# Optimization experiments

Hardware: AMD Instinct MI355X
Metric: run time of the kernel (lower is better)

The kernel has to match this reference:

```python
import jax, jax.numpy as jnp
import numpy as np

N, L, H, E, D = 8, 1024, 16, 1024, 64  # batch, seq_len, heads, embed_size, head_dim


def _xavier(k, shape):
    fan_out, fan_in = shape
    lim = np.sqrt(6.0 / (fan_in + fan_out)).astype(np.float32)
    return jax.random.uniform(k, shape, jnp.float32, -lim, lim)


def setup_inputs() -> dict:
    key = jax.random.key(0)
    ks = jax.random.split(key, 6)
    return {
        "x": jax.random.normal(ks[0], (N, L, E, 1), jnp.float32),
        "Wq": _xavier(ks[1], (D, D)), "bq": jnp.zeros((D,), jnp.float32),
        "Wk": _xavier(ks[2], (D, D)), "bk": jnp.zeros((D,), jnp.float32),
        "Wv": _xavier(ks[3], (D, D)), "bv": jnp.zeros((D,), jnp.float32),
        "Erel": jax.random.normal(ks[4], (1, L, D), jnp.float32),
        "Wo": _xavier(ks[5], (E, E)), "bo": jnp.zeros((E,), jnp.float32),
    }


def _skew(qe):
    # qe: [N, H, L, L] -> pad one zero col on the left, reshape, drop first row
    n, h, l, _ = qe.shape
    p = jnp.pad(qe, ((0, 0), (0, 0), (0, 0), (1, 0)))  # [N,H,L,L+1]
    p = p.reshape(n, h, l + 1, l)
    return p[:, :, 1:, :]  # [N,H,L,L]


def reference(x, Wq, bq, Wk, bk, Wv, bv, Erel, Wo, bo):
    x0 = x[:, :, :, 0]                      # [N, L, E]
    z = x0.reshape(N, L, H, D)              # [N, L, H, D]
    q = z @ Wq.T + bq
    k = z @ Wk.T + bk
    v = z @ Wv.T + bv
    # QE = queries.transpose(1,2) @ E.transpose(1,2): [N,H,L,D] @ [D,L] -> [N,H,L,L]
    QE = jnp.einsum('nlhd,td->nhlt', q, Erel[0])
    # mask_positions: zero where triu(ones,1).flip(1) == 1
    mask = jnp.flip(jnp.triu(jnp.ones((L, L), jnp.float32), 1), axis=1)
    QE = jnp.where(mask == 1, 0.0, QE)
    S = _skew(QE)                           # [N,H,L,L]
    qk = jnp.einsum('nqhd,nkhd->nhqk', q, k)
    attention = jax.nn.softmax(qk / jnp.sqrt(jnp.float32(E)), axis=3) + S
    out = jnp.einsum('nhql,nlhd->nqhd', attention, v).reshape(N, L, H * D)
    return out @ Wo.T + bo                  # [N, L, E]
```

## Files before the change

### kernel.cpp

```cpp
#include <hip/hip_runtime.h>
#include <math.h>

#define N_ 8
#define L_ 1024
#define H_ 16
#define E_ 1024
#define D_ 64

typedef __bf16 bf16x8 __attribute__((ext_vector_type(8)));
typedef __bf16 bf16x4 __attribute__((ext_vector_type(4)));
typedef float  f32x4  __attribute__((ext_vector_type(4)));

#define MFMA16(a, b, c) __builtin_amdgcn_mfma_f32_16x16x32_bf16((a), (b), (c), 0, 0, 0)

#define KSCALE 0.04508422002778011f

__global__ __launch_bounds__(256) void prep_kernel(
    const float* __restrict__ Wo, const float* __restrict__ Erel,
    __bf16* __restrict__ wobf, __bf16* __restrict__ erbf)
{
    const int idx = blockIdx.x * 256 + threadIdx.x;
    const float* src;
    __bf16* dst;
    int off;
    if (blockIdx.x < 1024) { src = Wo;   dst = wobf; off = idx * 4; }
    else                   { src = Erel; dst = erbf; off = (idx - 1024 * 256) * 4; }
    const float4 f = *(const float4*)(src + off);
    bf16x4 h;
    h[0] = (__bf16)f.x; h[1] = (__bf16)f.y; h[2] = (__bf16)f.z; h[3] = (__bf16)f.w;
    *(bf16x4*)(dst + off) = h;
}

__global__ __launch_bounds__(256) void qkv_kernel(
    const float* __restrict__ x,
    const float* __restrict__ Wq, const float* __restrict__ bq,
    const float* __restrict__ Wk, const float* __restrict__ bk,
    const float* __restrict__ Wv, const float* __restrict__ bv,
    __bf16* __restrict__ qo, __bf16* __restrict__ ko, __bf16* __restrict__ vo)
{
    const int t = threadIdx.x, w = t >> 6, lane = t & 63;
    const int quad = lane >> 4, l16 = lane & 15;
    const int m0 = blockIdx.x * 64;

    __shared__ __bf16 xs[64][72];
    __shared__ __bf16 wls[3][64][72];

    #pragma unroll
    for (int i = 0; i < 4; ++i) {
        const int idx = t + i * 256, row = idx >> 4, c4 = idx & 15;
        {
            const float4 f = *(const float4*)(x + (size_t)(m0 + row) * 64 + c4 * 4);
            bf16x4 hh; hh[0]=(__bf16)f.x; hh[1]=(__bf16)f.y; hh[2]=(__bf16)f.z; hh[3]=(__bf16)f.w;
            *(bf16x4*)&xs[row][c4 * 4] = hh;
        }
        {
            const float4 f = *(const float4*)(Wq + (size_t)row * 64 + c4 * 4);
            bf16x4 hh; hh[0]=(__bf16)f.x; hh[1]=(__bf16)f.y; hh[2]=(__bf16)f.z; hh[3]=(__bf16)f.w;
            *(bf16x4*)&wls[0][row][c4 * 4] = hh;
        }
        {
            const float4 f = *(const float4*)(Wk + (size_t)row * 64 + c4 * 4);
            bf16x4 hh; hh[0]=(__bf16)f.x; hh[1]=(__bf16)f.y; hh[2]=(__bf16)f.z; hh[3]=(__bf16)f.w;
            *(bf16x4*)&wls[1][row][c4 * 4] = hh;
        }
        {
            const float4 f = *(const float4*)(Wv + (size_t)row * 64 + c4 * 4);
            bf16x4 hh; hh[0]=(__bf16)f.x; hh[1]=(__bf16)f.y; hh[2]=(__bf16)f.z; hh[3]=(__bf16)f.w;
            *(bf16x4*)&wls[2][row][c4 * 4] = hh;
        }
    }
    __syncthreads();

    bf16x8 a[2];
    a[0] = *(const bf16x8*)&xs[w * 16 + l16][quad * 8];
    a[1] = *(const bf16x8*)&xs[w * 16 + l16][32 + quad * 8];

    f32x4 acc[12];
    const f32x4 zero4 = {0.f, 0.f, 0.f, 0.f};
    #pragma unroll
    for (int nt = 0; nt < 12; ++nt) acc[nt] = zero4;

    #pragma unroll
    for (int nt = 0; nt < 12; ++nt) {
        const int sel = nt >> 2, dt = nt & 3;
        #pragma unroll
        for (int c = 0; c < 2; ++c) {
            const bf16x8 b = *(const bf16x8*)&wls[sel][dt * 16 + l16][c * 32 + quad * 8];
            acc[nt] = MFMA16(a[c], b, acc[nt]);
        }
    }
    __syncthreads();

    __bf16* ts = &wls[0][0][0];
    const float* bias[3] = {bq, bk, bv};
    __bf16* outp[3] = {qo, ko, vo};
    #pragma unroll
    for (int nt = 0; nt < 12; ++nt) {
        const int sel = nt >> 2, dt = nt & 3;
        const float bb = bias[sel][dt * 16 + l16];
        const float scl = (sel == 1) ? KSCALE : 1.0f;
        #pragma unroll
        for (int r = 0; r < 4; ++r)
            ts[(size_t)(w * 16 + quad * 4 + r) * 208 + sel * 64 + dt * 16 + l16] =
                (__bf16)((acc[nt][r] + bb) * scl);
    }
    __syncthreads();
    #pragma unroll
    for (int sel = 0; sel < 3; ++sel)
        #pragma unroll
        for (int i = 0; i < 2; ++i) {
            const int idx = t * 2 + i, row = idx >> 3, c = idx & 7;
            *(float4*)(outp[sel] + (size_t)(m0 + row) * 64 + c * 8) =
                *(const float4*)&ts[(size_t)row * 208 + sel * 64 + c * 8];
        }
}

__global__ __launch_bounds__(256) void vtr_kernel(
    const __bf16* __restrict__ v, __bf16* __restrict__ vt)
{
    const int bid = blockIdx.x;
    const int lt = bid & 15, h = (bid >> 4) & 15, n = bid >> 8;
    const int l0 = lt * 64;
    const int t = threadIdx.x;
    __shared__ __bf16 ls[64][72];

    const int lrow = t & 63, c0 = t >> 6;
    #pragma unroll
    for (int i = 0; i < 2; ++i) {
        const int c = c0 + i * 4;
        union { float4 f; __bf16 hv[8]; } u;
        u.f = *(const float4*)(v + ((size_t)(n * L_ + l0 + lrow) * H_ + h) * D_ + c * 8);
        #pragma unroll
        for (int j = 0; j < 8; ++j) ls[c * 8 + j][lrow] = u.hv[j];
    }
    __syncthreads();
    const int drow0 = t >> 3, lc = t & 7;
    #pragma unroll
    for (int i = 0; i < 2; ++i) {
        const int d = drow0 + i * 32;
        *(float4*)(vt + ((size_t)(n * H_ + h) * D_ + d) * L_ + l0 + lc * 8) =
            *(const float4*)&ls[d][lc * 8];
    }
}

__global__ __launch_bounds__(512, 4) void attn_kernel(
    const __bf16* __restrict__ qbf, const __bf16* __restrict__ kbf,
    const __bf16* __restrict__ vtrb, const __bf16* __restrict__ erbf,
    __bf16* __restrict__ attnA)
{
    const int bid = blockIdx.x;
    const int p  = (bid & 7) | ((bid >> 6) << 3);
    const int qt = (bid >> 3) & 7;
    const int h = p & 15, n = p >> 4;
    const int q0 = qt * 128;
    const int t = threadIdx.x, w = t >> 6, lane = t & 63;
    const int quad = lane >> 4, l16 = lane & 15;

    __shared__ __bf16 ks[2][64][72];
    __shared__ __bf16 vt[2][64][72];
    __shared__ __bf16 ps[128][72];

    const int qw0 = q0 + w * 16;
    const size_t qrowoff = ((size_t)(n * L_ + qw0 + l16) * H_ + h) * D_;
    const bf16x8 qa0 = *(const bf16x8*)(qbf + qrowoff + quad * 8);
    const bf16x8 qa1 = *(const bf16x8*)(qbf + qrowoff + 32 + quad * 8);

    const __bf16* kbase = kbf + ((size_t)n * L_ * H_ + h) * D_;
    const __bf16* vbase = vtrb + ((size_t)(n * H_ + h) * D_) * L_;
    const int srow = t >> 3, sc8 = (t & 7) * 8;

    float4 kreg = *(const float4*)(kbase + (size_t)srow * 1024 + sc8);
    float4 vreg = *(const float4*)(vbase + (size_t)srow * 1024 + sc8);
    *(float4*)&ks[0][srow][sc8] = kreg;
    *(float4*)&vt[0][srow][sc8] = vreg;
    kreg = *(const float4*)(kbase + 64 * 1024 + (size_t)srow * 1024 + sc8);
    vreg = *(const float4*)(vbase + 64 + (size_t)srow * 1024 + sc8);
    __syncthreads();

    const f32x4 zero4 = {0.f, 0.f, 0.f, 0.f};
    f32x4 Os[4], Or[4];
    #pragma unroll
    for (int nt = 0; nt < 4; ++nt) { Os[nt] = zero4; Or[nt] = zero4; }
    float esum = 0.f;

    for (int kt = 0; kt < 16; ++kt) {
        const int cur = kt & 1;
        if (kt < 15) {
            *(float4*)&ks[cur ^ 1][srow][sc8] = kreg;
            *(float4*)&vt[cur ^ 1][srow][sc8] = vreg;
            if (kt < 14) {
                kreg = *(const float4*)(kbase + (size_t)(kt + 2) * 64 * 1024
                                        + (size_t)srow * 1024 + sc8);
                vreg = *(const float4*)(vbase + (kt + 2) * 64
                                        + (size_t)srow * 1024 + sc8);
            }
        }

        f32x4 sc[4];
        #pragma unroll
        for (int nt = 0; nt < 4; ++nt) {
            f32x4 acc = zero4;
            acc = MFMA16(*(const bf16x8*)&ks[cur][nt * 16 + l16][quad * 8], qa0, acc);
            acc = MFMA16(*(const bf16x8*)&ks[cur][nt * 16 + l16][32 + quad * 8], qa1, acc);
            sc[nt] = acc;
        }

        #pragma unroll
        for (int nt = 0; nt < 4; ++nt) {
            bf16x4 pk;
            #pragma unroll
            for (int r = 0; r < 4; ++r) {
                const float e = exp2f(sc[nt][r]);
                esum += e;
                pk[r] = (__bf16)e;
            }
            *(bf16x4*)&ps[w * 16 + l16][nt * 16 + quad * 4] = pk;
        }

        {
            const bf16x8 pb0 = *(const bf16x8*)&ps[w * 16 + l16][quad * 8];
            const bf16x8 pb1 = *(const bf16x8*)&ps[w * 16 + l16][32 + quad * 8];
            #pragma unroll
            for (int nt = 0; nt < 4; ++nt) {
                Os[nt] = MFMA16(*(const bf16x8*)&vt[cur][nt * 16 + l16][quad * 8], pb0, Os[nt]);
                Os[nt] = MFMA16(*(const bf16x8*)&vt[cur][nt * 16 + l16][32 + quad * 8], pb1, Os[nt]);
            }
        }

        if (kt * 64 <= qw0 + 15) {
            const int tb = kt * 64 + 1008 - qw0;
            #pragma unroll
            for (int st = 0; st < 5; ++st) {
                int tr = tb + st * 16 + l16;
                tr = tr > 1023 ? 1023 : tr;
                const __bf16* er = erbf + (size_t)tr * 64;
                f32x4 acc = zero4;
                acc = MFMA16(*(const bf16x8*)(er + quad * 8), qa0, acc);
                acc = MFMA16(*(const bf16x8*)(er + 32 + quad * 8), qa1, acc);
                #pragma unroll
                for (int r = 0; r < 4; ++r) {
                    const int kc = st * 16 + quad * 4 + r + l16 - 15;
                    const int tg = tb + st * 16 + quad * 4 + r;
                    if (kc >= 0 && kc < 64)
                        ps[w * 16 + l16][kc] = (tg <= 1023) ? (__bf16)acc[r]
                                                            : (__bf16)0.0f;
                }
            }
            const bf16x8 rb0 = *(const bf16x8*)&ps[w * 16 + l16][quad * 8];
            const bf16x8 rb1 = *(const bf16x8*)&ps[w * 16 + l16][32 + quad * 8];
            #pragma unroll
            for (int nt = 0; nt < 4; ++nt) {
                Or[nt] = MFMA16(*(const bf16x8*)&vt[cur][nt * 16 + l16][quad * 8], rb0, Or[nt]);
                Or[nt] = MFMA16(*(const bf16x8*)&vt[cur][nt * 16 + l16][32 + quad * 8], rb1, Or[nt]);
            }
        }
        __syncthreads();
    }

    esum += __shfl_xor(esum, 16, 64);
    esum += __shfl_xor(esum, 32, 64);
    const float invl = 1.0f / esum;
    #pragma unroll
    for (int nt = 0; nt < 4; ++nt) {
        bf16x4 ov;
        #pragma unroll
        for (int r = 0; r < 4; ++r)
            ov[r] = (__bf16)(Os[nt][r] * invl + Or[nt][r]);
        *(bf16x4*)&ps[w * 16 + l16][nt * 16 + quad * 4] = ov;
    }
    const int erow = lane >> 3, ec8 = lane & 7;
    #pragma unroll
    for (int i = 0; i < 2; ++i) {
        const int r = erow + i * 8;
        const float4 val = *(const float4*)&ps[w * 16 + r][ec8 * 8];
        *(float4*)(attnA + ((size_t)(n * L_ + qw0 + r)) * E_ + h * 64 + ec8 * 8) = val;
    }
}

__global__ __launch_bounds__(256) void proj_kernel(
    const __bf16* __restrict__ A, const __bf16* __restrict__ W,
    const float* __restrict__ bo, float* __restrict__ out)
{
    const int bid = blockIdx.x;
    const int rt = bid >> 3, ct = bid & 7;
    const int r0 = rt * 128, c0 = ct * 128;
    const int t = threadIdx.x, w = t >> 6, lane = t & 63;
    const int quad = lane >> 4, l16 = lane & 15;
    const int wm = w >> 1, wn = w & 1;

    __shared__ __bf16 As[128 * 64];
    __shared__ __bf16 Bs[128 * 64];

    f32x4 acc[16];
    const f32x4 zero4 = {0.f, 0.f, 0.f, 0.f};
    #pragma unroll
    for (int i = 0; i < 16; ++i) acc[i] = zero4;

    const int lrow = lane >> 3, lcg = lane & 7;

    for (int kt = 0; kt < 16; ++kt) {
        const int e0 = kt * 64;
        __syncthreads();
        #pragma unroll
        for (int i = 0; i < 4; ++i) {
            const int chunk = w * 4 + i;
            const int row = chunk * 8 + lrow;
            const __bf16* ga = A + (size_t)(r0 + row) * E_ + e0 + lcg * 8;
            const __bf16* gb = W + (size_t)(c0 + row) * E_ + e0 + lcg * 8;
            __builtin_amdgcn_global_load_lds(
                (const __attribute__((address_space(1))) void*)ga,
                (__attribute__((address_space(3))) void*)&As[chunk * 512], 16, 0, 0);
            __builtin_amdgcn_global_load_lds(
                (const __attribute__((address_space(1))) void*)gb,
                (__attribute__((address_space(3))) void*)&Bs[chunk * 512], 16, 0, 0);
        }
        __syncthreads();
        #pragma unroll
        for (int c = 0; c < 2; ++c) {
            bf16x8 am[4], bn[4];
            #pragma unroll
            for (int i = 0; i < 4; ++i) {
                am[i] = *(const bf16x8*)&As[(wm * 64 + i * 16 + l16) * 64 + c * 32 + quad * 8];
                bn[i] = *(const bf16x8*)&Bs[(wn * 64 + i * 16 + l16) * 64 + c * 32 + quad * 8];
            }
            #pragma unroll
            for (int i = 0; i < 4; ++i)
                #pragma unroll
                for (int j = 0; j < 4; ++j)
                    acc[i * 4 + j] = MFMA16(am[i], bn[j], acc[i * 4 + j]);
        }
    }

    #pragma unroll
    for (int i = 0; i < 4; ++i)
        #pragma unroll
        for (int j = 0; j < 4; ++j) {
            const int col = c0 + wn * 64 + j * 16 + l16;
            const float bb = bo[col];
            #pragma unroll
            for (int r = 0; r < 4; ++r)
                out[(size_t)(r0 + wm * 64 + i * 16 + quad * 4 + r) * E_ + col] =
                    acc[i * 4 + j][r] + bb;
        }
}

extern "C" void kernel_launch(void* const* d_in, const int* in_sizes, int n_in,
                              void* d_out, int out_size, void* d_ws, size_t ws_size,
                              hipStream_t stream)
{
    const float* x    = (const float*)d_in[0];
    const float* Wq   = (const float*)d_in[1];
    const float* bq   = (const float*)d_in[2];
    const float* Wk   = (const float*)d_in[3];
    const float* bk   = (const float*)d_in[4];
    const float* Wv   = (const float*)d_in[5];
    const float* bv   = (const float*)d_in[6];
    const float* Erel = (const float*)d_in[7];
    const float* Wo   = (const float*)d_in[8];
    const float* bo   = (const float*)d_in[9];
    float* out = (float*)d_out;

    char* p = (char*)d_ws;
    __bf16* qbf   = (__bf16*)p; p += (size_t)N_ * L_ * H_ * D_ * 2;
    __bf16* kbf   = (__bf16*)p; p += (size_t)N_ * L_ * H_ * D_ * 2;
    __bf16* vbf   = (__bf16*)p; p += (size_t)N_ * L_ * H_ * D_ * 2;
    __bf16* vtrb  = (__bf16*)p; p += (size_t)N_ * L_ * H_ * D_ * 2;
    __bf16* attnA = (__bf16*)p; p += (size_t)N_ * L_ * E_ * 2;
    __bf16* wobf  = (__bf16*)p; p += (size_t)E_ * E_ * 2;
    __bf16* erbf  = (__bf16*)p; p += (size_t)L_ * D_ * 2;

    prep_kernel<<<1088, 256, 0, stream>>>(Wo, Erel, wobf, erbf);
    qkv_kernel<<<(N_ * L_ * H_) / 64, 256, 0, stream>>>(x, Wq, bq, Wk, bk, Wv, bv,
                                                        qbf, kbf, vbf);
    vtr_kernel<<<N_ * H_ * (L_ / 64), 256, 0, stream>>>(vbf, vtrb);
    attn_kernel<<<N_ * H_ * (L_ / 128), 512, 0, stream>>>(qbf, kbf, vtrb, erbf, attnA);
    proj_kernel<<<(N_ * L_ / 128) * (E_ / 128), 256, 0, stream>>>(attnA, wobf, bo, out);
}
```

Baseline: 312.2 us.

## Split relative-position term into separate kernel and double query rows per block

```diff
diff --git a/kernel.cpp b/kernel.cpp
--- a/kernel.cpp
+++ b/kernel.cpp
@@ -143,16 +143,156 @@
     }
 }
 
-__global__ __launch_bounds__(512, 4) void attn_kernel(
+__global__ __launch_bounds__(512, 4) void rel_kernel(
+    const __bf16* __restrict__ qbf, const __bf16* __restrict__ vtrb,
+    const __bf16* __restrict__ erbf, __bf16* __restrict__ rbuf)
+{
+    const int bid = blockIdx.x;
+    const int qt = 3 - (bid >> 7);
+    const int p = bid & 127;
+    const int h = p & 15, n = p >> 4;
+    const int q0 = qt * 256;
+    const int t = threadIdx.x, w = t >> 6, lane = t & 63;
+    const int quad = lane >> 4, l16 = lane & 15;
+
+    __shared__ __bf16 vt[2][64][72];
+    __shared__ __bf16 rs[128][72];
+
+    const int qA = q0 + w * 16;
+    const size_t qoffA = ((size_t)(n * L_ + qA + l16) * H_ + h) * D_;
+    const size_t qoffB = qoffA + (size_t)128 * H_ * D_;
+    const bf16x8 qaA0 = *(const bf16x8*)(qbf + qoffA + quad * 8);
+    const bf16x8 qaA1 = *(const bf16x8*)(qbf + qoffA + 32 + quad * 8);
+    const bf16x8 qaB0 = *(const bf16x8*)(qbf + qoffB + quad * 8);
+    const bf16x8 qaB1 = *(const bf16x8*)(qbf + qoffB + 32 + quad * 8);
+
+    const __bf16* vbase = vtrb + ((size_t)(n * H_ + h) * D_) * L_;
+    const int srow = t >> 3, sc8 = (t & 7) * 8;
+    const int ktmax = qt * 4 + 4;
+
+    float4 vreg = *(const float4*)(vbase + (size_t)srow * 1024 + sc8);
+    *(float4*)&vt[0][srow][sc8] = vreg;
+    vreg = *(const float4*)(vbase + 64 + (size_t)srow * 1024 + sc8);
+    __syncthreads();
+
+    const f32x4 zero4 = {0.f, 0.f, 0.f, 0.f};
+    f32x4 OrA[4], OrB[4];
+    #pragma unroll
+    for (int nt = 0; nt < 4; ++nt) { OrA[nt] = zero4; OrB[nt] = zero4; }
+
+    for (int kt = 0; kt < ktmax; ++kt) {
+        const int cur = kt & 1;
+        if (kt + 1 < ktmax) {
+            *(float4*)&vt[cur ^ 1][srow][sc8] = vreg;
+            if (kt + 2 < ktmax)
+                vreg = *(const float4*)(vbase + (kt + 2) * 64
+                                        + (size_t)srow * 1024 + sc8);
+        }
+
+        const bool dorelA = (kt * 64 <= qA + 15);
+        const bool dorelB = (kt * 64 <= qA + 128 + 15);
+        bf16x8 rbA0, rbA1, rbB0, rbB1;
+
+        if (dorelA) {
+            const int tb = kt * 64 + 1008 - qA;
+            #pragma unroll
+            for (int st = 0; st < 5; ++st) {
+                int tr = tb + st * 16 + l16;
+                tr = tr > 1023 ? 1023 : tr;
+                const __bf16* er = erbf + (size_t)tr * 64;
+                f32x4 acc = zero4;
+                acc = MFMA16(*(const bf16x8*)(er + quad * 8), qaA0, acc);
+                acc = MFMA16(*(const bf16x8*)(er + 32 + quad * 8), qaA1, acc);
+                #pragma unroll
+                for (int r = 0; r < 4; ++r) {
+                    const int kc = st * 16 + quad * 4 + r + l16 - 15;
+                    const int tg = tb + st * 16 + quad * 4 + r;
+                    if (kc >= 0 && kc < 64)
+                        rs[w * 16 + l16][kc] = (tg <= 1023) ? (__bf16)acc[r]
+                                                            : (__bf16)0.0f;
+                }
+            }
+            rbA0 = *(const bf16x8*)&rs[w * 16 + l16][quad * 8];
+            rbA1 = *(const bf16x8*)&rs[w * 16 + l16][32 + quad * 8];
+        }
+        if (dorelB) {
+            const int tb = kt * 64 + 1008 - (qA + 128);
+            #pragma unroll
+            for (int st = 0; st < 5; ++st) {
+                int tr = tb + st * 16 + l16;
+                tr = tr > 1023 ? 1023 : tr;
+                const __bf16* er = erbf + (size_t)tr * 64;
+                f32x4 acc = zero4;
+                acc = MFMA16(*(const bf16x8*)(er + quad * 8), qaB0, acc);
+                acc = MFMA16(*(const bf16x8*)(er + 32 + quad * 8), qaB1, acc);
+                #pragma unroll
+                for (int r = 0; r < 4; ++r) {
+                    const int kc = st * 16 + quad * 4 + r + l16 - 15;
+                    const int tg = tb + st * 16 + quad * 4 + r;
+                    if (kc >= 0 && kc < 64)
+                        rs[w * 16 + l16][kc] = (tg <= 1023) ? (__bf16)acc[r]
+                                                            : (__bf16)0.0f;
+                }
+            }
+            rbB0 = *(const bf16x8*)&rs[w * 16 + l16][quad * 8];
+            rbB1 = *(const bf16x8*)&rs[w * 16 + l16][32 + quad * 8];
+        }
+
+        #pragma unroll
+        for (int nt = 0; nt < 4; ++nt) {
+            const bf16x8 va0 = *(const bf16x8*)&vt[cur][nt * 16 + l16][quad * 8];
+            const bf16x8 va1 = *(const bf16x8*)&vt[cur][nt * 16 + l16][32 + quad * 8];
+            if (dorelA) {
+                OrA[nt] = MFMA16(va0, rbA0, OrA[nt]);
+                OrA[nt] = MFMA16(va1, rbA1, OrA[nt]);
+            }
+            if (dorelB) {
+                OrB[nt] = MFMA16(va0, rbB0, OrB[nt]);
+                OrB[nt] = MFMA16(va1, rbB1, OrB[nt]);
+            }
+        }
+        __syncthreads();
+    }
+
+    const int erow = lane >> 3, ec8 = lane & 7;
+    #pragma unroll
+    for (int nt = 0; nt < 4; ++nt) {
+        bf16x4 ov;
+        #pragma unroll
+        for (int r = 0; r < 4; ++r) ov[r] = (__bf16)OrA[nt][r];
+        *(bf16x4*)&rs[w * 16 + l16][nt * 16 + quad * 4] = ov;
+    }
+    #pragma unroll
+    for (int i = 0; i < 2; ++i) {
+        const int r = erow + i * 8;
+        *(float4*)(rbuf + ((size_t)(n * L_ + qA + r)) * E_ + h * 64 + ec8 * 8) =
+            *(const float4*)&rs[w * 16 + r][ec8 * 8];
+    }
+    #pragma unroll
+    for (int nt = 0; nt < 4; ++nt) {
+        bf16x4 ov;
+        #pragma unroll
+        for (int r = 0; r < 4; ++r) ov[r] = (__bf16)OrB[nt][r];
+        *(bf16x4*)&rs[w * 16 + l16][nt * 16 + quad * 4] = ov;
+    }
+    #pragma unroll
+    for (int i = 0; i < 2; ++i) {
+        const int r = erow + i * 8;
+        *(float4*)(rbuf + ((size_t)(n * L_ + qA + 128 + r)) * E_ + h * 64 + ec8 * 8) =
+            *(const float4*)&rs[w * 16 + r][ec8 * 8];
+    }
+}
+
+__global__ __launch_bounds__(512, 4) void flash_kernel(
     const __bf16* __restrict__ qbf, const __bf16* __restrict__ kbf,
-    const __bf16* __restrict__ vtrb, const __bf16* __restrict__ erbf,
+    const __bf16* __restrict__ vtrb, const __bf16* __restrict__ rbuf,
     __bf16* __restrict__ attnA)
 {
     const int bid = blockIdx.x;
-    const int p  = (bid & 7) | ((bid >> 6) << 3);
-    const int qt = (bid >> 3) & 7;
+    const int qt = bid >> 7;
+    const int p = bid & 127;
     const int h = p & 15, n = p >> 4;
-    const int q0 = qt * 128;
+    const int q0 = qt * 256;
     const int t = threadIdx.x, w = t >> 6, lane = t & 63;
     const int quad = lane >> 4, l16 = lane & 15;
 
@@ -160,10 +300,13 @@
     __shared__ __bf16 vt[2][64][72];
     __shared__ __bf16 ps[128][72];
 
-    const int qw0 = q0 + w * 16;
-    const size_t qrowoff = ((size_t)(n * L_ + qw0 + l16) * H_ + h) * D_;
-    const bf16x8 qa0 = *(const bf16x8*)(qbf + qrowoff + quad * 8);
-    const bf16x8 qa1 = *(const bf16x8*)(qbf + qrowoff + 32 + quad * 8);
+    const int qA = q0 + w * 16;
+    const size_t qoffA = ((size_t)(n * L_ + qA + l16) * H_ + h) * D_;
+    const size_t qoffB = qoffA + (size_t)128 * H_ * D_;
+    const bf16x8 qaA0 = *(const bf16x8*)(qbf + qoffA + quad * 8);
+    const bf16x8 qaA1 = *(const bf16x8*)(qbf + qoffA + 32 + quad * 8);
+    const bf16x8 qaB0 = *(const bf16x8*)(qbf + qoffB + quad * 8);
+    const bf16x8 qaB1 = *(const bf16x8*)(qbf + qoffB + 32 + quad * 8);
 
     const __bf16* kbase = kbf + ((size_t)n * L_ * H_ + h) * D_;
     const __bf16* vbase = vtrb + ((size_t)(n * H_ + h) * D_) * L_;
@@ -178,10 +321,10 @@
     __syncthreads();
 
     const f32x4 zero4 = {0.f, 0.f, 0.f, 0.f};
-    f32x4 Os[4], Or[4];
-    #pragma unroll
-    for (int nt = 0; nt < 4; ++nt) { Os[nt] = zero4; Or[nt] = zero4; }
-    float esum = 0.f;
+    f32x4 OsA[4], OsB[4];
+    #pragma unroll
+    for (int nt = 0; nt < 4; ++nt) { OsA[nt] = zero4; OsB[nt] = zero4; }
+    float esumA = 0.f, esumB = 0.f;
 
     for (int kt = 0; kt < 16; ++kt) {
         const int cur = kt & 1;
@@ -196,13 +339,19 @@
             }
         }
 
-        f32x4 sc[4];
+        f32x4 sA[4], sB[4];
         #pragma unroll
         for (int nt = 0; nt < 4; ++nt) {
-            f32x4 acc = zero4;
-            acc = MFMA16(*(const bf16x8*)&ks[cur][nt * 16 + l16][quad * 8], qa0, acc);
-            acc = MFMA16(*(const bf16x8*)&ks[cur][nt * 16 + l16][32 + quad * 8], qa1, acc);
-            sc[nt] = acc;
+            const bf16x8 ka0 = *(const bf16x8*)&ks[cur][nt * 16 + l16][quad * 8];
+            const bf16x8 ka1 = *(const bf16x8*)&ks[cur][nt * 16 + l16][32 + quad * 8];
+            f32x4 a = zero4;
+            a = MFMA16(ka0, qaA0, a);
+            a = MFMA16(ka1, qaA1, a);
+            sA[nt] = a;
+            f32x4 b = zero4;
+            b = MFMA16(ka0, qaB0, b);
+            b = MFMA16(ka1, qaB1, b);
+            sB[nt] = b;
         }
 
         #pragma unroll
@@ -210,70 +359,85 @@
             bf16x4 pk;
             #pragma unroll
             for (int r = 0; r < 4; ++r) {
-                const float e = exp2f(sc[nt][r]);
-                esum += e;
+                const float e = exp2f(sA[nt][r]);
+                esumA += e;
                 pk[r] = (__bf16)e;
             }
             *(bf16x4*)&ps[w * 16 + l16][nt * 16 + quad * 4] = pk;
         }
-
-        {
-            const bf16x8 pb0 = *(const bf16x8*)&ps[w * 16 + l16][quad * 8];
-            const bf16x8 pb1 = *(const bf16x8*)&ps[w * 16 + l16][32 + quad * 8];
-            #pragma unroll
-            for (int nt = 0; nt < 4; ++nt) {
-                Os[nt] = MFMA16(*(const bf16x8*)&vt[cur][nt * 16 + l16][quad * 8], pb0, Os[nt]);
-                Os[nt] = MFMA16(*(const bf16x8*)&vt[cur][nt * 16 + l16][32 + quad * 8], pb1, Os[nt]);
-            }
-        }
-
-        if (kt * 64 <= qw0 + 15) {
-            const int tb = kt * 64 + 1008 - qw0;
-            #pragma unroll
-            for (int st = 0; st < 5; ++st) {
-                int tr = tb + st * 16 + l16;
-                tr = tr > 1023 ? 1023 : tr;
-                const __bf16* er = erbf + (size_t)tr * 64;
-                f32x4 acc = zero4;
-                acc = MFMA16(*(const bf16x8*)(er + quad * 8), qa0, acc);
-                acc = MFMA16(*(const bf16x8*)(er + 32 + quad * 8), qa1, acc);
-                #pragma unroll
-                for (int r = 0; r < 4; ++r) {
-                    const int kc = st * 16 + quad * 4 + r + l16 - 15;
-                    const int tg = tb + st * 16 + quad * 4 + r;
-                    if (kc >= 0 && kc < 64)
-                        ps[w * 16 + l16][kc] = (tg <= 1023) ? (__bf16)acc[r]
-                                                            : (__bf16)0.0f;
-                }
-            }
-            const bf16x8 rb0 = *(const bf16x8*)&ps[w * 16 + l16][quad * 8];
-            const bf16x8 rb1 = *(const bf16x8*)&ps[w * 16 + l16][32 + quad * 8];
-            #pragma unroll
-            for (int nt = 0; nt < 4; ++nt) {
-                Or[nt] = MFMA16(*(const bf16x8*)&vt[cur][nt * 16 + l16][quad * 8], rb0, Or[nt]);
-                Or[nt] = MFMA16(*(const bf16x8*)&vt[cur][nt * 16 + l16][32 + quad * 8], rb1, Or[nt]);
-            }
+        const bf16x8 pbA0 = *(const bf16x8*)&ps[w * 16 + l16][quad * 8];
+        const bf16x8 pbA1 = *(const bf16x8*)&ps[w * 16 + l16][32 + quad * 8];
+        #pragma unroll
+        for (int nt = 0; nt < 4; ++nt) {
+            bf16x4 pk;
+            #pragma unroll
+            for (int r = 0; r < 4; ++r) {
+                const float e = exp2f(sB[nt][r]);
+                esumB += e;
+                pk[r] = (__bf16)e;
+            }
+            *(bf16x4*)&ps[w * 16 + l16][nt * 16 + quad * 4] = pk;
+        }
+        const bf16x8 pbB0 = *(const bf16x8*)&ps[w * 16 + l16][quad * 8];
+        const bf16x8 pbB1 = *(const bf16x8*)&ps[w * 16 + l16][32 + quad * 8];
+
+        #pragma unroll
+        for (int nt = 0; nt < 4; ++nt) {
+            const bf16x8 va0 = *(const bf16x8*)&vt[cur][nt * 16 + l16][quad * 8];
+            const bf16x8 va1 = *(const bf16x8*)&vt[cur][nt * 16 + l16][32 + quad * 8];
+            OsA[nt] = MFMA16(va0, pbA0, OsA[nt]);
+            OsA[nt] = MFMA16(va1, pbA1, OsA[nt]);
+            OsB[nt] = MFMA16(va0, pbB0, OsB[nt]);
+            OsB[nt] = MFMA16(va1, pbB1, OsB[nt]);
         }
         __syncthreads();
     }
 
-    esum += __shfl_xor(esum, 16, 64);
-    esum += __shfl_xor(esum, 32, 64);
-    const float invl = 1.0f / esum;
+    esumA += __shfl_xor(esumA, 16, 64);
+    esumA += __shfl_xor(esumA, 32, 64);
+    esumB += __shfl_xor(esumB, 16, 64);
+    esumB += __shfl_xor(esumB, 32, 64);
+    const float invlA = 1.0f / esumA;
+    const float invlB = 1.0f / esumB;
+    const int erow = lane >> 3, ec8 = lane & 7;
+
     #pragma unroll
     for (int nt = 0; nt < 4; ++nt) {
         bf16x4 ov;
         #pragma unroll
-        for (int r = 0; r < 4; ++r)
-            ov[r] = (__bf16)(Os[nt][r] * invl + Or[nt][r]);
+        for (int r = 0; r < 4; ++r) ov[r] = (__bf16)(OsA[nt][r] * invlA);
         *(bf16x4*)&ps[w * 16 + l16][nt * 16 + quad * 4] = ov;
     }
-    const int erow = lane >> 3, ec8 = lane & 7;
     #pragma unroll
     for (int i = 0; i < 2; ++i) {
         const int r = erow + i * 8;
-        const float4 val = *(const float4*)&ps[w * 16 + r][ec8 * 8];
-        *(float4*)(attnA + ((size_t)(n * L_ + qw0 + r)) * E_ + h * 64 + ec8 * 8) = val;
+        const size_t goff = ((size_t)(n * L_ + qA + r)) * E_ + h * 64 + ec8 * 8;
+        union { float4 f; __bf16 hv[8]; } ua, ub, uo;
+        ua.f = *(const float4*)&ps[w * 16 + r][ec8 * 8];
+        ub.f = *(const float4*)(rbuf + goff);
+        #pragma unroll
+        for (int j = 0; j < 8; ++j)
+            uo.hv[j] = (__bf16)((float)ua.hv[j] + (float)ub.hv[j]);
+        *(float4*)(attnA + goff) = uo.f;
+    }
+    #pragma unroll
+    for (int nt = 0; nt < 4; ++nt) {
+        bf16x4 ov;
+        #pragma unroll
+        for (int r = 0; r < 4; ++r) ov[r] = (__bf16)(OsB[nt][r] * invlB);
+        *(bf16x4*)&ps[w * 16 + l16][nt * 16 + quad * 4] = ov;
+    }
+    #pragma unroll
+    for (int i = 0; i < 2; ++i) {
+        const int r = erow + i * 8;
+        const size_t goff = ((size_t)(n * L_ + qA + 128 + r)) * E_ + h * 64 + ec8 * 8;
+        union { float4 f; __bf16 hv[8]; } ua, ub, uo;
+        ua.f = *(const float4*)&ps[w * 16 + r][ec8 * 8];
+        ub.f = *(const float4*)(rbuf + goff);
+        #pragma unroll
+        for (int j = 0; j < 8; ++j)
+            uo.hv[j] = (__bf16)((float)ua.hv[j] + (float)ub.hv[j]);
+        *(float4*)(attnA + goff) = uo.f;
     }
 }
 
@@ -366,6 +530,7 @@
     __bf16* vbf   = (__bf16*)p; p += (size_t)N_ * L_ * H_ * D_ * 2;
     __bf16* vtrb  = (__bf16*)p; p += (size_t)N_ * L_ * H_ * D_ * 2;
     __bf16* attnA = (__bf16*)p; p += (size_t)N_ * L_ * E_ * 2;
+    __bf16* rbuf  = (__bf16*)p; p += (size_t)N_ * L_ * E_ * 2;
     __bf16* wobf  = (__bf16*)p; p += (size_t)E_ * E_ * 2;
     __bf16* erbf  = (__bf16*)p; p += (size_t)L_ * D_ * 2;
 
@@ -373,6 +538,7 @@
     qkv_kernel<<<(N_ * L_ * H_) / 64, 256, 0, stream>>>(x, Wq, bq, Wk, bk, Wv, bv,
                                                         qbf, kbf, vbf);
     vtr_kernel<<<N_ * H_ * (L_ / 64), 256, 0, stream>>>(vbf, vtrb);
-    attn_kernel<<<N_ * H_ * (L_ / 128), 512, 0, stream>>>(qbf, kbf, vtrb, erbf, attnA);
+    rel_kernel<<<512, 512, 0, stream>>>(qbf, vtrb, erbf, rbuf);
+    flash_kernel<<<512, 512, 0, stream>>>(qbf, kbf, vtrb, rbuf, attnA);
     proj_kernel<<<(N_ * L_ / 128) * (E_ / 128), 256, 0, stream>>>(attnA, wobf, bo, out);
 }
```

Measured after the change: 303.5 us. 1.03x faster.

## Process two query sub-tiles per attention block to reuse K/V tiles

Applied to the files above, without the earlier changes.

```diff
diff --git a/kernel.cpp b/kernel.cpp
--- a/kernel.cpp
+++ b/kernel.cpp
@@ -149,10 +149,10 @@
     __bf16* __restrict__ attnA)
 {
     const int bid = blockIdx.x;
-    const int p  = (bid & 7) | ((bid >> 6) << 3);
-    const int qt = (bid >> 3) & 7;
+    const int qt = 3 - (bid >> 7);
+    const int p = bid & 127;
     const int h = p & 15, n = p >> 4;
-    const int q0 = qt * 128;
+    const int q0 = qt * 256;
     const int t = threadIdx.x, w = t >> 6, lane = t & 63;
     const int quad = lane >> 4, l16 = lane & 15;
 
@@ -160,10 +160,13 @@
     __shared__ __bf16 vt[2][64][72];
     __shared__ __bf16 ps[128][72];
 
-    const int qw0 = q0 + w * 16;
-    const size_t qrowoff = ((size_t)(n * L_ + qw0 + l16) * H_ + h) * D_;
-    const bf16x8 qa0 = *(const bf16x8*)(qbf + qrowoff + quad * 8);
-    const bf16x8 qa1 = *(const bf16x8*)(qbf + qrowoff + 32 + quad * 8);
+    const int qA = q0 + w * 16;
+    const size_t qoffA = ((size_t)(n * L_ + qA + l16) * H_ + h) * D_;
+    const size_t qoffB = qoffA + (size_t)128 * H_ * D_;
+    const bf16x8 qaA0 = *(const bf16x8*)(qbf + qoffA + quad * 8);
+    const bf16x8 qaA1 = *(const bf16x8*)(qbf + qoffA + 32 + quad * 8);
+    const bf16x8 qaB0 = *(const bf16x8*)(qbf + qoffB + quad * 8);
+    const bf16x8 qaB1 = *(const bf16x8*)(qbf + qoffB + 32 + quad * 8);
 
     const __bf16* kbase = kbf + ((size_t)n * L_ * H_ + h) * D_;
     const __bf16* vbase = vtrb + ((size_t)(n * H_ + h) * D_) * L_;
@@ -178,10 +181,12 @@
     __syncthreads();
 
     const f32x4 zero4 = {0.f, 0.f, 0.f, 0.f};
-    f32x4 Os[4], Or[4];
-    #pragma unroll
-    for (int nt = 0; nt < 4; ++nt) { Os[nt] = zero4; Or[nt] = zero4; }
-    float esum = 0.f;
+    f32x4 OsA[4], OsB[4], OrA[4], OrB[4];
+    #pragma unroll
+    for (int nt = 0; nt < 4; ++nt) {
+        OsA[nt] = zero4; OsB[nt] = zero4; OrA[nt] = zero4; OrB[nt] = zero4;
+    }
+    float esumA = 0.f, esumB = 0.f;
 
     for (int kt = 0; kt < 16; ++kt) {
         const int cur = kt & 1;
@@ -196,47 +201,62 @@
             }
         }
 
-        f32x4 sc[4];
         #pragma unroll
         for (int nt = 0; nt < 4; ++nt) {
-            f32x4 acc = zero4;
-            acc = MFMA16(*(const bf16x8*)&ks[cur][nt * 16 + l16][quad * 8], qa0, acc);
-            acc = MFMA16(*(const bf16x8*)&ks[cur][nt * 16 + l16][32 + quad * 8], qa1, acc);
-            sc[nt] = acc;
-        }
+            const bf16x8 ka0 = *(const bf16x8*)&ks[cur][nt * 16 + l16][quad * 8];
+            const bf16x8 ka1 = *(const bf16x8*)&ks[cur][nt * 16 + l16][32 + quad * 8];
+            f32x4 a = zero4;
+            a = MFMA16(ka0, qaA0, a);
+            a = MFMA16(ka1, qaA1, a);
+            bf16x4 pk;
+            #pragma unroll
+            for (int r = 0; r < 4; ++r) pk[r] = (__bf16)exp2f(a[r]);
+            *(bf16x4*)&ps[w * 16 + l16][nt * 16 + quad * 4] = pk;
+        }
+        const bf16x8 pbA0 = *(const bf16x8*)&ps[w * 16 + l16][quad * 8];
+        const bf16x8 pbA1 = *(const bf16x8*)&ps[w * 16 + l16][32 + quad * 8];
 
         #pragma unroll
         for (int nt = 0; nt < 4; ++nt) {
+            const bf16x8 ka0 = *(const bf16x8*)&ks[cur][nt * 16 + l16][quad * 8];
+            const bf16x8 ka1 = *(const bf16x8*)&ks[cur][nt * 16 + l16][32 + quad * 8];
+            f32x4 b = zero4;
+            b = MFMA16(ka0, qaB0, b);
+            b = MFMA16(ka1, qaB1, b);
             bf16x4 pk;
             #pragma unroll
-            for (int r = 0; r < 4; ++r) {
-                const float e = exp2f(sc[nt][r]);
-                esum += e;
-                pk[r] = (__bf16)e;
-            }
+            for (int r = 0; r < 4; ++r) pk[r] = (__bf16)exp2f(b[r]);
             *(bf16x4*)&ps[w * 16 + l16][nt * 16 + quad * 4] = pk;
         }
-
-        {
-            const bf16x8 pb0 = *(const bf16x8*)&ps[w * 16 + l16][quad * 8];
-            const bf16x8 pb1 = *(const bf16x8*)&ps[w * 16 + l16][32 + quad * 8];
-            #pragma unroll
-            for (int nt = 0; nt < 4; ++nt) {
-                Os[nt] = MFMA16(*(const bf16x8*)&vt[cur][nt * 16 + l16][quad * 8], pb0, Os[nt]);
-                Os[nt] = MFMA16(*(const bf16x8*)&vt[cur][nt * 16 + l16][32 + quad * 8], pb1, Os[nt]);
-            }
-        }
-
-        if (kt * 64 <= qw0 + 15) {
-            const int tb = kt * 64 + 1008 - qw0;
+        const bf16x8 pbB0 = *(const bf16x8*)&ps[w * 16 + l16][quad * 8];
+        const bf16x8 pbB1 = *(const bf16x8*)&ps[w * 16 + l16][32 + quad * 8];
+
+        #pragma unroll
+        for (int j = 0; j < 8; ++j) {
+            esumA += (float)pbA0[j] + (float)pbA1[j];
+            esumB += (float)pbB0[j] + (float)pbB1[j];
+        }
+
+        #pragma unroll
+        for (int nt = 0; nt < 4; ++nt) {
+            const bf16x8 va0 = *(const bf16x8*)&vt[cur][nt * 16 + l16][quad * 8];
+            const bf16x8 va1 = *(const bf16x8*)&vt[cur][nt * 16 + l16][32 + quad * 8];
+            OsA[nt] = MFMA16(va0, pbA0, OsA[nt]);
+            OsA[nt] = MFMA16(va1, pbA1, OsA[nt]);
+            OsB[nt] = MFMA16(va0, pbB0, OsB[nt]);
+            OsB[nt] = MFMA16(va1, pbB1, OsB[nt]);
+        }
+
+        if (kt * 64 <= qA + 15) {
+            const int tb = kt * 64 + 1008 - qA;
             #pragma unroll
             for (int st = 0; st < 5; ++st) {
                 int tr = tb + st * 16 + l16;
                 tr = tr > 1023 ? 1023 : tr;
                 const __bf16* er = erbf + (size_t)tr * 64;
                 f32x4 acc = zero4;
-                acc = MFMA16(*(const bf16x8*)(er + quad * 8), qa0, acc);
-                acc = MFMA16(*(const bf16x8*)(er + 32 + quad * 8), qa1, acc);
+                acc = MFMA16(*(const bf16x8*)(er + quad * 8), qaA0, acc);
+                acc = MFMA16(*(const bf16x8*)(er + 32 + quad * 8), qaA1, acc);
                 #pragma unroll
                 for (int r = 0; r < 4; ++r) {
                     const int kc = st * 16 + quad * 4 + r + l16 - 15;
@@ -250,30 +270,79 @@
             const bf16x8 rb1 = *(const bf16x8*)&ps[w * 16 + l16][32 + quad * 8];
             #pragma unroll
             for (int nt = 0; nt < 4; ++nt) {
-                Or[nt] = MFMA16(*(const bf16x8*)&vt[cur][nt * 16 + l16][quad * 8], rb0, Or[nt]);
-                Or[nt] = MFMA16(*(const bf16x8*)&vt[cur][nt * 16 + l16][32 + quad * 8], rb1, Or[nt]);
+                const bf16x8 va0 = *(const bf16x8*)&vt[cur][nt * 16 + l16][quad * 8];
+                const bf16x8 va1 = *(const bf16x8*)&vt[cur][nt * 16 + l16][32 + quad * 8];
+                OrA[nt] = MFMA16(va0, rb0, OrA[nt]);
+                OrA[nt] = MFMA16(va1, rb1, OrA[nt]);
+            }
+        }
+        if (kt * 64 <= qA + 143) {
+            const int tb = kt * 64 + 1008 - (qA + 128);
+            #pragma unroll
+            for (int st = 0; st < 5; ++st) {
+                int tr = tb + st * 16 + l16;
+                tr = tr > 1023 ? 1023 : tr;
+                const __bf16* er = erbf + (size_t)tr * 64;
+                f32x4 acc = zero4;
+                acc = MFMA16(*(const bf16x8*)(er + quad * 8), qaB0, acc);
+                acc = MFMA16(*(const bf16x8*)(er + 32 + quad * 8), qaB1, acc);
+                #pragma unroll
+                for (int r = 0; r < 4; ++r) {
+                    const int kc = st * 16 + quad * 4 + r + l16 - 15;
+                    const int tg = tb + st * 16 + quad * 4 + r;
+                    if (kc >= 0 && kc < 64)
+                        ps[w * 16 + l16][kc] = (tg <= 1023) ? (__bf16)acc[r]
+                                                            : (__bf16)0.0f;
+                }
+            }
+            const bf16x8 rb0 = *(const bf16x8*)&ps[w * 16 + l16][quad * 8];
+            const bf16x8 rb1 = *(const bf16x8*)&ps[w * 16 + l16][32 + quad * 8];
+            #pragma unroll
+            for (int nt = 0; nt < 4; ++nt) {
+                const bf16x8 va0 = *(const bf16x8*)&vt[cur][nt * 16 + l16][quad * 8];
+                const bf16x8 va1 = *(const bf16x8*)&vt[cur][nt * 16 + l16][32 + quad * 8];
+                OrB[nt] = MFMA16(va0, rb0, OrB[nt]);
+                OrB[nt] = MFMA16(va1, rb1, OrB[nt]);
             }
         }
         __syncthreads();
     }
 
-    esum += __shfl_xor(esum, 16, 64);
-    esum += __shfl_xor(esum, 32, 64);
-    const float invl = 1.0f / esum;
+    esumA += __shfl_xor(esumA, 16, 64);
+    esumA += __shfl_xor(esumA, 32, 64);
+    esumB += __shfl_xor(esumB, 16, 64);
+    esumB += __shfl_xor(esumB, 32, 64);
+    const float invlA = 1.0f / esumA;
+    const float invlB = 1.0f / esumB;
+    const int erow = lane >> 3, ec8 = lane & 7;
+
     #pragma unroll
     for (int nt = 0; nt < 4; ++nt) {
         bf16x4 ov;
         #pragma unroll
         for (int r = 0; r < 4; ++r)
-            ov[r] = (__bf16)(Os[nt][r] * invl + Or[nt][r]);
+            ov[r] = (__bf16)(OsA[nt][r] * invlA + OrA[nt][r]);
         *(bf16x4*)&ps[w * 16 + l16][nt * 16 + quad * 4] = ov;
     }
-    const int erow = lane >> 3, ec8 = lane & 7;
     #pragma unroll
     for (int i = 0; i < 2; ++i) {
         const int r = erow + i * 8;
-        const float4 val = *(const float4*)&ps[w * 16 + r][ec8 * 8];
-        *(float4*)(attnA + ((size_t)(n * L_ + qw0 + r)) * E_ + h * 64 + ec8 * 8) = val;
+        *(float4*)(attnA + ((size_t)(n * L_ + qA + r)) * E_ + h * 64 + ec8 * 8) =
+            *(const float4*)&ps[w * 16 + r][ec8 * 8];
+    }
+    #pragma unroll
+    for (int nt = 0; nt < 4; ++nt) {
+        bf16x4 ov;
+        #pragma unroll
+        for (int r = 0; r < 4; ++r)
+            ov[r] = (__bf16)(OsB[nt][r] * invlB + OrB[nt][r]);
+        *(bf16x4*)&ps[w * 16 + l16][nt * 16 + quad * 4] = ov;
+    }
+    #pragma unroll
+    for (int i = 0; i < 2; ++i) {
+        const int r = erow + i * 8;
+        *(float4*)(attnA + ((size_t)(n * L_ + qA + 128 + r)) * E_ + h * 64 + ec8 * 8) =
+            *(const float4*)&ps[w * 16 + r][ec8 * 8];
     }
 }
 
@@ -373,6 +442,6 @@
     qkv_kernel<<<(N_ * L_ * H_) / 64, 256, 0, stream>>>(x, Wq, bq, Wk, bk, Wv, bv,
                                                         qbf, kbf, vbf);
     vtr_kernel<<<N_ * H_ * (L_ / 64), 256, 0, stream>>>(vbf, vtrb);
-    attn_kernel<<<N_ * H_ * (L_ / 128), 512, 0, stream>>>(qbf, kbf, vtrb, erbf, attnA);
+    attn_kernel<<<512, 512, 0, stream>>>(qbf, kbf, vtrb, erbf, attnA);
     proj_kernel<<<(N_ * L_ / 128) * (E_ / 128), 256, 0, stream>>>(attnA, wobf, bo, out);
 }
```

Result: slower. 359.1 us (+15.0%).

## Single-buffer K/V tiles, share V fragments across both PV products, reverse q-tile order

Applied to the files above, without the earlier changes.

```diff
diff --git a/kernel.cpp b/kernel.cpp
--- a/kernel.cpp
+++ b/kernel.cpp
@@ -150,14 +150,14 @@
 {
     const int bid = blockIdx.x;
     const int p  = (bid & 7) | ((bid >> 6) << 3);
-    const int qt = (bid >> 3) & 7;
+    const int qt = 7 - ((bid >> 3) & 7);
     const int h = p & 15, n = p >> 4;
     const int q0 = qt * 128;
     const int t = threadIdx.x, w = t >> 6, lane = t & 63;
     const int quad = lane >> 4, l16 = lane & 15;
 
-    __shared__ __bf16 ks[2][64][72];
-    __shared__ __bf16 vt[2][64][72];
+    __shared__ __bf16 ks[64][72];
+    __shared__ __bf16 vt[64][72];
     __shared__ __bf16 ps[128][72];
 
     const int qw0 = q0 + w * 16;
@@ -171,8 +171,8 @@
 
     float4 kreg = *(const float4*)(kbase + (size_t)srow * 1024 + sc8);
     float4 vreg = *(const float4*)(vbase + (size_t)srow * 1024 + sc8);
-    *(float4*)&ks[0][srow][sc8] = kreg;
-    *(float4*)&vt[0][srow][sc8] = vreg;
+    *(float4*)&ks[srow][sc8] = kreg;
+    *(float4*)&vt[srow][sc8] = vreg;
     kreg = *(const float4*)(kbase + 64 * 1024 + (size_t)srow * 1024 + sc8);
     vreg = *(const float4*)(vbase + 64 + (size_t)srow * 1024 + sc8);
     __syncthreads();
@@ -184,24 +184,12 @@
     float esum = 0.f;
 
     for (int kt = 0; kt < 16; ++kt) {
-        const int cur = kt & 1;
-        if (kt < 15) {
-            *(float4*)&ks[cur ^ 1][srow][sc8] = kreg;
-            *(float4*)&vt[cur ^ 1][srow][sc8] = vreg;
-            if (kt < 14) {
-                kreg = *(const float4*)(kbase + (size_t)(kt + 2) * 64 * 1024
-                                        + (size_t)srow * 1024 + sc8);
-                vreg = *(const float4*)(vbase + (kt + 2) * 64
-                                        + (size_t)srow * 1024 + sc8);
-            }
-        }
-
         f32x4 sc[4];
         #pragma unroll
         for (int nt = 0; nt < 4; ++nt) {
             f32x4 acc = zero4;
-            acc = MFMA16(*(const bf16x8*)&ks[cur][nt * 16 + l16][quad * 8], qa0, acc);
-            acc = MFMA16(*(const bf16x8*)&ks[cur][nt * 16 + l16][32 + quad * 8], qa1, acc);
+            acc = MFMA16(*(const bf16x8*)&ks[nt * 16 + l16][quad * 8], qa0, acc);
+            acc = MFMA16(*(const bf16x8*)&ks[nt * 16 + l16][32 + quad * 8], qa1, acc);
             sc[nt] = acc;
         }
 
@@ -216,18 +204,12 @@
             }
             *(bf16x4*)&ps[w * 16 + l16][nt * 16 + quad * 4] = pk;
         }
-
-        {
-            const bf16x8 pb0 = *(const bf16x8*)&ps[w * 16 + l16][quad * 8];
-            const bf16x8 pb1 = *(const bf16x8*)&ps[w * 16 + l16][32 + quad * 8];
-            #pragma unroll
-            for (int nt = 0; nt < 4; ++nt) {
-                Os[nt] = MFMA16(*(const bf16x8*)&vt[cur][nt * 16 + l16][quad * 8], pb0, Os[nt]);
-                Os[nt] = MFMA16(*(const bf16x8*)&vt[cur][nt * 16 + l16][32 + quad * 8], pb1, Os[nt]);
-            }
-        }
-
-        if (kt * 64 <= qw0 + 15) {
+        const bf16x8 pb0 = *(const bf16x8*)&ps[w * 16 + l16][quad * 8];
+        const bf16x8 pb1 = *(const bf16x8*)&ps[w * 16 + l16][32 + quad * 8];
+
+        const bool dorel = (kt * 64 <= qw0 + 15);
+        bf16x8 rb0{}, rb1{};
+        if (dorel) {
             const int tb = kt * 64 + 1008 - qw0;
             #pragma unroll
             for (int st = 0; st < 5; ++st) {
@@ -246,15 +228,34 @@
                                                             : (__bf16)0.0f;
                 }
             }
-            const bf16x8 rb0 = *(const bf16x8*)&ps[w * 16 + l16][quad * 8];
-            const bf16x8 rb1 = *(const bf16x8*)&ps[w * 16 + l16][32 + quad * 8];
-            #pragma unroll
-            for (int nt = 0; nt < 4; ++nt) {
-                Or[nt] = MFMA16(*(const bf16x8*)&vt[cur][nt * 16 + l16][quad * 8], rb0, Or[nt]);
-                Or[nt] = MFMA16(*(const bf16x8*)&vt[cur][nt * 16 + l16][32 + quad * 8], rb1, Or[nt]);
-            }
-        }
-        __syncthreads();
+            rb0 = *(const bf16x8*)&ps[w * 16 + l16][quad * 8];
+            rb1 = *(const bf16x8*)&ps[w * 16 + l16][32 + quad * 8];
+        }
+
+        #pragma unroll
+        for (int nt = 0; nt < 4; ++nt) {
+            const bf16x8 va0 = *(const bf16x8*)&vt[nt * 16 + l16][quad * 8];
+            const bf16x8 va1 = *(const bf16x8*)&vt[nt * 16 + l16][32 + quad * 8];
+            Os[nt] = MFMA16(va0, pb0, Os[nt]);
+            Os[nt] = MFMA16(va1, pb1, Os[nt]);
+            if (dorel) {
+                Or[nt] = MFMA16(va0, rb0, Or[nt]);
+                Or[nt] = MFMA16(va1, rb1, Or[nt]);
+            }
+        }
+
+        if (kt < 15) {
+            __syncthreads();
+            *(float4*)&ks[srow][sc8] = kreg;
+            *(float4*)&vt[srow][sc8] = vreg;
+            __syncthreads();
+            if (kt < 14) {
+                kreg = *(const float4*)(kbase + (size_t)(kt + 2) * 64 * 1024
+                                        + (size_t)srow * 1024 + sc8);
+                vreg = *(const float4*)(vbase + (kt + 2) * 64
+                                        + (size_t)srow * 1024 + sc8);
+            }
+        }
     }
 
     esum += __shfl_xor(esum, 16, 64);
```

Result: slower. 702.8 us (+125.2%).
